# Kernel tuning notes

Hardware: AMD Instinct MI355X
Metric: run time of the kernel (lower is better)

Reference implementation:

```python
import jax, jax.numpy as jnp
import numpy as np

B, H, W, C = 8, 32, 32, 512
NUM_HEADS = 8
NUM_GROUPS = 32
EPS = 1e-5
SKIP_SCALE = 1.0
HEAD_DIM = C // NUM_HEADS


def setup_inputs() -> dict:
    key = jax.random.key(0)
    ks = jax.random.split(key, 7)
    fan_in, fan_out = C, 3 * C
    lim_qkv = np.sqrt(6.0 / (fan_in + fan_out))
    lim_out = 1e-5 * np.sqrt(6.0 / (C + C))
    return {
        "x": jax.random.normal(ks[0], (B, H, W, C), jnp.float32),
        "norm_scale": jnp.ones((C,), jnp.float32),
        "norm_bias": jnp.zeros((C,), jnp.float32),
        "qkv_kernel": jax.random.uniform(ks[1], (C, NUM_HEADS, 3 * HEAD_DIM), jnp.float32, -lim_qkv, lim_qkv),
        "qkv_bias": jnp.zeros((NUM_HEADS, 3 * HEAD_DIM), jnp.float32),
        "out_kernel": jax.random.uniform(ks[2], (NUM_HEADS, HEAD_DIM, C), jnp.float32, -lim_out, lim_out),
        "out_bias": jnp.zeros((C,), jnp.float32),
    }


def group_norm(x, scale, bias):
    # x: (B, S, C); normalize per-group over (S, C//G), flax GroupNorm semantics
    b, s, c = x.shape
    g = NUM_GROUPS
    xg = x.reshape(b, s, g, c // g)
    mean = jnp.mean(xg, axis=(1, 3), keepdims=True)
    var = jnp.var(xg, axis=(1, 3), keepdims=True)
    xg = (xg - mean) * jax.lax.rsqrt(var + EPS)
    return xg.reshape(b, s, c) * scale + bias


def reference(x, norm_scale, norm_bias, qkv_kernel, qkv_bias, out_kernel, out_bias):
    batch_dims = x.shape[:-3]
    h, w, c = x.shape[-3:]
    xi = x.reshape(-1, h * w, c)  # (B, S, C)
    out = group_norm(xi, norm_scale, norm_bias)
    # QKV projection: (B,S,C) x (C, NH, 3*HD) -> (B,S,NH,3*HD)
    qkv = jnp.einsum('bsc,chd->bshd', out, qkv_kernel) + qkv_bias
    q, k, v = jnp.split(qkv, 3, axis=-1)  # each (B,S,NH,HD)
    scale = 1.0 / jnp.sqrt(jnp.sqrt(jnp.asarray(HEAD_DIM, jnp.float32)))
    q = q * scale
    k = k * scale
    attn = jnp.einsum('bqhd,bkhd->bhqk', q, k)
    attn = jax.nn.softmax(attn, axis=-1)
    o = jnp.einsum('bhqk,bkhd->bqhd', attn, v)
    o = jnp.einsum('bqhd,hdc->bqc', o, out_kernel) + out_bias
    o = (o + xi) * SKIP_SCALE
    return o.reshape((*batch_dims, h, w, c))
```

## Files before the change

kernel.cpp:

```cpp
#include <hip/hip_runtime.h>
#include <stdint.h>

typedef __attribute__((ext_vector_type(8))) short short8;
typedef __attribute__((ext_vector_type(4))) float f32x4;
typedef __attribute__((ext_vector_type(16))) float f32x16;
typedef __attribute__((ext_vector_type(4))) unsigned int u32x4;
typedef unsigned short u16;
typedef unsigned int u32;

#define NBATCH 8
#define SLEN 1024
#define CDIM 512
#define NHEADS 8
#define HDIM 64
#define MROWS (NBATCH*SLEN)
#define NQKV (NHEADS*3*HDIM)
#define QK_SCALE 0.35355339059327373f
#define Q_SCALE_L2E 0.18033688011111793f
#define DEFER_THR 11.541560327111707f

__device__ inline u16 f2bf(float f){
  union{float f; uint32_t i;} v; v.f=f;
  uint32_t r = v.i + 0x7fffu + ((v.i>>16)&1u);
  return (u16)(r>>16);
}

__device__ inline u32 pk2(float a, float b){
  u32 r;
  asm("v_cvt_pk_bf16_f32 %0, %1, %2" : "=v"(r) : "v"(a), "v"(b));
  return r;
}

__device__ inline float exp2r(float x){
  float r;
  asm("v_exp_f32 %0, %1" : "=v"(r) : "v"(x));
  return r;
}

__device__ __forceinline__ void gld16(const u16* g, u16* l){
  __builtin_amdgcn_global_load_lds(
    (const __attribute__((address_space(1))) void*)g,
    (__attribute__((address_space(3))) void*)l, 16, 0, 0);
}

__device__ __forceinline__ void prep_body(const float* __restrict__ w, u16* __restrict__ wt,
                                          int N, int blk, int t){
  int tk = blk / (N/64), tn = blk % (N/64);
  int k0 = tk*64, n0 = tn*64;
  __shared__ u16 lt[64][72];
  int row = t >> 2, slot = t & 3;
  const float* src = w + (size_t)(k0+row)*N + n0 + slot*16;
  #pragma unroll
  for (int j=0;j<16;++j)
    lt[row][slot*16+j] = f2bf(src[j]);
  __syncthreads();
  u16 tmp[16];
  #pragma unroll
  for (int j=0;j<16;++j) tmp[j] = lt[slot*16+j][row];
  *(u32x4*)(wt + (size_t)(n0+row)*512 + k0 + slot*16)     = *(u32x4*)tmp;
  *(u32x4*)(wt + (size_t)(n0+row)*512 + k0 + slot*16 + 8) = *(u32x4*)(tmp+8);
}

__global__ __launch_bounds__(256) void prep_all(const float* __restrict__ wqkv, const float* __restrict__ wout,
                                                u16* __restrict__ wqkv_t, u16* __restrict__ wout_t){
  int blk = blockIdx.x, t = threadIdx.x;
  if (blk < 8*(NQKV/64)) prep_body(wqkv, wqkv_t, NQKV, blk, t);
  else                   prep_body(wout, wout_t, CDIM, blk - 8*(NQKV/64), t);
}

__global__ __launch_bounds__(512, 2) void gn_fused(const float* __restrict__ x,
                        const float* __restrict__ scale, const float* __restrict__ bias,
                        u16* __restrict__ xn){
  int bid = blockIdx.x;
  int b = bid >> 5, g = bid & 31;
  int t = threadIdx.x;
  const float* base = x + (size_t)b*SLEN*CDIM + g*16;
  u16* obase = xn + (size_t)b*SLEN*CDIM + g*16;
  float s1=0.f, s2=0.f;
  for (int s = t; s < SLEN; s += 512){
    const float4* p = (const float4*)(base + (size_t)s*CDIM);
    #pragma unroll
    for (int j=0;j<4;++j){
      float4 v = p[j];
      s1 += v.x+v.y+v.z+v.w;
      s2 += v.x*v.x + v.y*v.y + v.z*v.z + v.w*v.w;
    }
  }
  #pragma unroll
  for (int m=1;m<64;m<<=1){ s1 += __shfl_xor(s1,m); s2 += __shfl_xor(s2,m); }
  __shared__ float red[16];
  __shared__ float mv[2];
  int wid = t>>6;
  if ((t&63)==0){ red[wid*2]=s1; red[wid*2+1]=s2; }
  __syncthreads();
  if (t==0){
    float a=0,c=0;
    #pragma unroll
    for (int w2=0;w2<8;++w2){ a+=red[w2*2]; c+=red[w2*2+1]; }
    float mean = a*(1.f/16384.f);
    float var  = c*(1.f/16384.f) - mean*mean;
    mv[0] = mean; mv[1] = rsqrtf(var + 1e-5f);
  }
  __syncthreads();
  float mean = mv[0], rstd = mv[1];
  float sc[16], bi[16];
  #pragma unroll
  for (int j=0;j<16;++j){ sc[j] = scale[g*16+j]*rstd; bi[j] = bias[g*16+j] - mean*scale[g*16+j]*rstd; }
  for (int s = t; s < SLEN; s += 512){
    const float* xp = base + (size_t)s*CDIM;
    short8 o0, o1;
    #pragma unroll
    for (int j=0;j<16;++j){
      float v = xp[j]*sc[j] + bi[j];
      if (j<8) o0[j] = (short)f2bf(v); else o1[j-8] = (short)f2bf(v);
    }
    short8* dst = (short8*)(obase + (size_t)s*CDIM);
    dst[0]=o0; dst[1]=o1;
  }
}

#define BM 128
#define BN 128
#define BK 64

template<int EPI, int NT>
__global__ __launch_bounds__(256, 3) void gemm_bf16(
    const u16* __restrict__ A, const u16* __restrict__ Bt,
    const float* __restrict__ bias, const float* __restrict__ resid,
    float* __restrict__ outF,
    u16* __restrict__ qb, u16* __restrict__ kb, u16* __restrict__ vtb)
{
  const int K = CDIM;
  int t = threadIdx.x;
  int l = t & 63, wid = t >> 6;
  int g = l >> 4, c = l & 15;
  int wr = wid >> 1, wc = wid & 1;
  int nwg = gridDim.x;
  int cpx = nwg >> 3;
  int orig = blockIdx.x;
  int swz = (orig & 7)*cpx + (orig >> 3);
  int m0 = (swz / NT) * BM, n0 = (swz % NT) * BN;

  __shared__ __attribute__((aligned(16))) u16 ls[16384];
  char* lsAc = (char*)ls; char* lsBc = (char*)(ls + 8192);

  f32x4 acc[4][4];
  #pragma unroll
  for (int i=0;i<4;++i)
    #pragma unroll
    for(int j=0;j<4;++j) acc[i][j] = (f32x4)0.f;

  int lrow = l >> 3, slot = l & 7;
  int scol = ((slot ^ lrow) << 3);
  const int KT = K / BK;
  for (int kt=0; kt<KT; ++kt){
    __syncthreads();
    int kbo = kt*BK;
    #pragma unroll
    for (int q2=0; q2<4; ++q2){
      int row = wid*32 + q2*8 + lrow;
      gld16(A  + (size_t)(m0+row)*K + kbo + scol, ls        + (wid*4+q2)*512);
      gld16(Bt + (size_t)(n0+row)*K + kbo + scol, ls + 8192 + (wid*4+q2)*512);
    }
    asm volatile("s_waitcnt vmcnt(0)" ::: "memory");
    __syncthreads();
    #pragma unroll
    for (int kk=0; kk<2; ++kk){
      short8 af[4], bfr[4];
      #pragma unroll
      for (int i=0;i<4;++i){
        int rowA = wr*64 + i*16 + c;
        af[i]  = *(const short8*)(lsAc + rowA*128 + ((kk*4+g) ^ (rowA&7))*16);
        int rowB = wc*64 + i*16 + c;
        bfr[i] = *(const short8*)(lsBc + rowB*128 + ((kk*4+g) ^ (rowB&7))*16);
      }
      #pragma unroll
      for (int i=0;i<4;++i)
        #pragma unroll
        for (int j=0;j<4;++j)
          acc[i][j] = __builtin_amdgcn_mfma_f32_16x16x32_bf16(af[i], bfr[j], acc[i][j], 0,0,0);
    }
  }

  if (EPI == 0){
    int b = m0 >> 10, s0 = m0 & (SLEN-1);
    __syncthreads();
    u16* lsC = ls;
    #pragma unroll
    for (int i=0;i<4;++i){
      int rl0 = wr*64 + i*16 + g*4;
      #pragma unroll
      for (int j=0;j<4;++j){
        int cl = wc*64 + j*16 + c;
        int gcol = n0 + cl;
        int jj = gcol % 192;
        float sc_ = (jj < 64) ? Q_SCALE_L2E : 1.0f;
        float bv = bias[gcol];
        #pragma unroll
        for (int r=0;r<4;++r)
          lsC[(rl0+r)*128 + cl] = f2bf((acc[i][j][r] + bv)*sc_);
      }
    }
    __syncthreads();
    #pragma unroll
    for (int cc=0; cc<8; ++cc){
      int ch = cc*256 + t;
      int rl = ch >> 4, slot2 = ch & 15;
      int cl = slot2*8;
      int gcol = n0 + cl;
      int h = gcol / 192, jj = gcol % 192;
      int s = s0 + rl;
      u32x4 vv = *(const u32x4*)(lsC + rl*128 + cl);
      size_t rowb = ((size_t)(b*NHEADS+h))*SLEN + s;
      if (jj < 64)       __builtin_nontemporal_store(vv, (u32x4*)(qb + rowb*HDIM + jj));
      else if (jj < 128) __builtin_nontemporal_store(vv, (u32x4*)(kb + rowb*HDIM + (jj-64)));
    }
    int blk3 = (n0 >> 7) % 3;
    if (blk3 != 0){
      __syncthreads();
      u16* lsV = ls;
      #pragma unroll
      for (int i=0;i<4;++i){
        int rl0 = wr*64 + i*16 + g*4;
        #pragma unroll
        for (int j=0;j<4;++j){
          int cl = wc*64 + j*16 + c;
          int jj = (n0 + cl) % 192;
          if (jj >= 128){
            #pragma unroll
            for (int r=0;r<4;++r)
              lsV[(jj-128)*136 + rl0 + r] = f2bf(acc[i][j][r] + bias[n0+cl]);
          }
        }
      }
      __syncthreads();
      int hv = (n0 + ((blk3==1)?0:64)) / 192;
      size_t vbase = ((size_t)(b*NHEADS+hv))*HDIM*SLEN;
      #pragma unroll
      for (int cc=0; cc<4; ++cc){
        int chunk = cc*256 + t;
        int d = chunk >> 4, so = (chunk & 15)*8;
        u32x4 vv = *(const u32x4*)(lsV + d*136 + so);
        __builtin_nontemporal_store(vv, (u32x4*)(vtb + vbase + (size_t)d*SLEN + s0 + so));
      }
    }
  } else {
    #pragma unroll
    for (int i=0;i<4;++i){
      int grow = m0 + wr*64 + i*16 + g*4;
      #pragma unroll
      for (int j=0;j<4;++j){
        int gcol = n0 + wc*64 + j*16 + c;
        float bv = bias[gcol];
        #pragma unroll
        for (int r=0;r<4;++r){
          size_t off = (size_t)(grow+r)*CDIM + gcol;
          float rv = __builtin_nontemporal_load(&resid[off]);
          __builtin_nontemporal_store(acc[i][j][r] + bv + rv, &outF[off]);
        }
      }
    }
  }
}

#define PV_KS(PT, QOFF, V0, V1, KS, OA, OB) { \
    u32 A0 = pk2(PT[QOFF+0], PT[QOFF+1]); \
    u32 A1 = pk2(PT[QOFF+2], PT[QOFF+3]); \
    u32 B0 = pk2(PT[QOFF+4], PT[QOFF+5]); \
    u32 B1 = pk2(PT[QOFF+6], PT[QOFF+7]); \
    auto r0_ = __builtin_amdgcn_permlane32_swap((int)A0, (int)B0, false, false); \
    auto r1_ = __builtin_amdgcn_permlane32_swap((int)A1, (int)B1, false, false); \
    uint4 w; \
    w.x = (u32)r0_[0]; w.y = (u32)r1_[0]; w.z = (u32)r0_[1]; w.w = (u32)r1_[1]; \
    short8 fP; __builtin_memcpy(&fP, &w, 16); \
    OA = __builtin_amdgcn_mfma_f32_32x32x16_bf16(V0[KS], fP, OA, 0,0,0); \
    OB = __builtin_amdgcn_mfma_f32_32x32x16_bf16(V1[KS], fP, OB, 0,0,0); }

__global__ __launch_bounds__(256, 2) void attn_fused(const u16* __restrict__ qg,
  const u16* __restrict__ kg, const u16* __restrict__ vtg, u16* __restrict__ og)
{
  int bid = blockIdx.x;
  int nid = (bid & 7)*64 + (bid >> 3);
  int bh = nid >> 3, qi = nid & 7;
  int t = threadIdx.x, l = t & 63, wid = t >> 6;
  int q = l & 31, hi = l >> 5;
  int q0 = qi*128 + wid*32;

  __shared__ __attribute__((aligned(16))) u16 kl[4][4096];
  __shared__ __attribute__((aligned(16))) u16 vl[4][4096];

  const u16* qrow = qg + ((size_t)bh*SLEN + q0 + q)*HDIM + hi*8;
  short8 fQ[4];
  #pragma unroll
  for (int ds=0; ds<4; ++ds) fQ[ds] = *(const short8*)(qrow + ds*16);

  f32x16 o0a, o0b, o1a, o1b;
  #pragma unroll
  for (int r=0;r<16;++r){ o0a[r]=0.f; o0b[r]=0.f; o1a[r]=0.f; o1b[r]=0.f; }
  float mr = -1e30f, lsum = 0.f;

  const u16* kt_base = kg  + (size_t)bh*SLEN*HDIM;
  const u16* vt_base = vtg + (size_t)bh*HDIM*SLEN;
  int srow = l >> 3, sslot = l & 7;
  int scol8 = ((sslot ^ srow) << 3);

#define STAGE(BUF, KV) { \
    _Pragma("unroll") \
    for (int j=0;j<2;++j){ \
      int row = wid*16 + j*8 + srow; \
      int chunk = wid*2 + j; \
      gld16(kt_base + (size_t)((KV)*64 + row)*HDIM + scol8, &kl[BUF][chunk*512]); \
      gld16(vt_base + (size_t)row*SLEN + (KV)*64 + scol8,   &vl[BUF][chunk*512]); \
    } }

  STAGE(0, 0)
  STAGE(1, 1)
  STAGE(2, 2)
  STAGE(3, 3)

  int sl_q = q & 7;
  for (int p=0; p<8; ++p){
    if (p < 7) asm volatile("s_waitcnt vmcnt(8)" ::: "memory");
    else       asm volatile("s_waitcnt vmcnt(0)" ::: "memory");
    __syncthreads();
    int tA = 2*p, tB = 2*p+1;
    const u16* kA = &kl[tA&3][0]; const u16* kB = &kl[tB&3][0];
    const u16* vA = &vl[tA&3][0]; const u16* vB = &vl[tB&3][0];
    short8 fKA0[4], fKA1[4], fKB0[4], fKB1[4];
    #pragma unroll
    for (int ds=0; ds<4; ++ds){
      int sl = ((ds*2+hi) ^ sl_q) << 3;
      fKA0[ds] = *(const short8*)(kA + q*64 + sl);
      fKA1[ds] = *(const short8*)(kA + (q+32)*64 + sl);
      fKB0[ds] = *(const short8*)(kB + q*64 + sl);
      fKB1[ds] = *(const short8*)(kB + (q+32)*64 + sl);
    }
    f32x16 pA0, pA1, pB0, pB1;
    #pragma unroll
    for (int r=0;r<16;++r){ pA0[r]=0.f; pA1[r]=0.f; pB0[r]=0.f; pB1[r]=0.f; }
    __builtin_amdgcn_s_setprio(1);
    #pragma unroll
    for (int ds=0; ds<4; ++ds){
      pA0 = __builtin_amdgcn_mfma_f32_32x32x16_bf16(fKA0[ds], fQ[ds], pA0, 0,0,0);
      pB0 = __builtin_amdgcn_mfma_f32_32x32x16_bf16(fKB0[ds], fQ[ds], pB0, 0,0,0);
      pA1 = __builtin_amdgcn_mfma_f32_32x32x16_bf16(fKA1[ds], fQ[ds], pA1, 0,0,0);
      pB1 = __builtin_amdgcn_mfma_f32_32x32x16_bf16(fKB1[ds], fQ[ds], pB1, 0,0,0);
    }
    __builtin_amdgcn_s_setprio(0);
    short8 fVA0[4], fVA1[4], fVB0[4], fVB1[4];
    #pragma unroll
    for (int ks=0; ks<4; ++ks){
      int sl = ((ks*2+hi) ^ sl_q) << 3;
      fVA0[ks] = *(const short8*)(vA + q*64 + sl);
      fVA1[ks] = *(const short8*)(vA + (q+32)*64 + sl);
      fVB0[ks] = *(const short8*)(vB + q*64 + sl);
      fVB1[ks] = *(const short8*)(vB + (q+32)*64 + sl);
    }
    float a8[8];
    #pragma unroll
    for (int r=0;r<8;++r){
      float ma = fmaxf(fmaxf(pA0[r],pA0[r+8]), fmaxf(pA1[r],pA1[r+8]));
      float mb = fmaxf(fmaxf(pB0[r],pB0[r+8]), fmaxf(pB1[r],pB1[r+8]));
      a8[r] = fmaxf(ma, mb);
    }
    #pragma unroll
    for (int s=4;s>0;s>>=1)
      #pragma unroll
      for (int r=0;r<4;++r) if (r<s) a8[r] = fmaxf(a8[r], a8[r+s]);
    auto rm_ = __builtin_amdgcn_permlane32_swap(
        __builtin_bit_cast(int, a8[0]), __builtin_bit_cast(int, a8[0]), false, false);
    float tmax = fmaxf(a8[0], fmaxf(__builtin_bit_cast(float, rm_[0]),
                                    __builtin_bit_cast(float, rm_[1])));
    if (!__all(tmax <= mr + DEFER_THR)){
      float mn = fmaxf(mr, tmax);
      float alpha = exp2r(mr - mn);
      mr = mn;
      lsum *= alpha;
      #pragma unroll
      for (int r=0;r<16;++r){ o0a[r]*=alpha; o0b[r]*=alpha; o1a[r]*=alpha; o1b[r]*=alpha; }
    }
    #pragma unroll
    for (int r=0;r<16;++r){
      pA0[r] = exp2r(pA0[r]-mr); pA1[r] = exp2r(pA1[r]-mr);
      pB0[r] = exp2r(pB0[r]-mr); pB1[r] = exp2r(pB1[r]-mr);
    }
    float s8[8];
    #pragma unroll
    for (int r=0;r<8;++r)
      s8[r] = ((pA0[r]+pA0[r+8]) + (pA1[r]+pA1[r+8]))
            + ((pB0[r]+pB0[r+8]) + (pB1[r]+pB1[r+8]));
    #pragma unroll
    for (int s=4;s>0;s>>=1)
      #pragma unroll
      for (int r=0;r<4;++r) if (r<s) s8[r] += s8[r+s];
    auto rs_ = __builtin_amdgcn_permlane32_swap(
        __builtin_bit_cast(int, s8[0]), __builtin_bit_cast(int, s8[0]), false, false);
    lsum += __builtin_bit_cast(float, rs_[0]) + __builtin_bit_cast(float, rs_[1]);
    __builtin_amdgcn_s_setprio(1);
    PV_KS(pA0, 0, fVA0, fVA1, 0, o0a, o1a)
    PV_KS(pA0, 8, fVA0, fVA1, 1, o0a, o1a)
    PV_KS(pA1, 0, fVA0, fVA1, 2, o0b, o1b)
    PV_KS(pA1, 8, fVA0, fVA1, 3, o0b, o1b)
    PV_KS(pB0, 0, fVB0, fVB1, 0, o0a, o1a)
    PV_KS(pB0, 8, fVB0, fVB1, 1, o0a, o1a)
    PV_KS(pB1, 0, fVB0, fVB1, 2, o0b, o1b)
    PV_KS(pB1, 8, fVB0, fVB1, 3, o0b, o1b)
    __builtin_amdgcn_s_setprio(0);
    __syncthreads();
    if (p < 6){
      STAGE((2*p+4)&3, 2*p+4)
      STAGE((2*p+5)&3, 2*p+5)
    }
  }

  float inv = 1.f / lsum;
  int b = bh >> 3, h = bh & 7;
  u16* obase = og + ((size_t)b*SLEN + q0 + q)*CDIM + h*HDIM;
  #pragma unroll
  for (int pr=0; pr<8; ++pr){
    int d = ((2*pr)&3) + 8*(pr>>1) + 4*hi;
    *(u32*)(obase + d)      = pk2((o0a[2*pr]+o0b[2*pr])*inv, (o0a[2*pr+1]+o0b[2*pr+1])*inv);
    *(u32*)(obase + 32 + d) = pk2((o1a[2*pr]+o1b[2*pr])*inv, (o1a[2*pr+1]+o1b[2*pr+1])*inv);
  }
}

extern "C" void kernel_launch(void* const* d_in, const int* in_sizes, int n_in,
                              void* d_out, int out_size, void* d_ws, size_t ws_size,
                              hipStream_t stream){
  const float* x      = (const float*)d_in[0];
  const float* nscale = (const float*)d_in[1];
  const float* nbias  = (const float*)d_in[2];
  const float* wqkv   = (const float*)d_in[3];
  const float* bqkv   = (const float*)d_in[4];
  const float* wout   = (const float*)d_in[5];
  const float* bout   = (const float*)d_in[6];
  float* out = (float*)d_out;

  char* ws = (char*)d_ws;
  size_t off = 0;
  auto alloc = [&](size_t bytes){ void* p = ws + off; off += (bytes + 255) & ~255ull; return p; };
  u16* wqkv_t = (u16*)alloc((size_t)NQKV*CDIM*2);
  u16* wout_t = (u16*)alloc((size_t)CDIM*CDIM*2);
  u16* xn     = (u16*)alloc((size_t)MROWS*CDIM*2);
  u16* qb     = (u16*)alloc((size_t)MROWS*CDIM*2);
  u16* kb     = (u16*)alloc((size_t)MROWS*CDIM*2);
  u16* vtb    = (u16*)alloc((size_t)MROWS*CDIM*2);
  u16* ob     = (u16*)alloc((size_t)MROWS*CDIM*2);

  prep_all<<<dim3(8*(NQKV/64) + 8*(CDIM/64)), dim3(256), 0, stream>>>(wqkv, wout, wqkv_t, wout_t);
  gn_fused<<<dim3(256), dim3(512), 0, stream>>>(x, nscale, nbias, xn);
  gemm_bf16<0,12><<<dim3(768), dim3(256), 0, stream>>>(xn, wqkv_t, bqkv, nullptr, nullptr, qb, kb, vtb);
  attn_fused<<<dim3(512), dim3(256), 0, stream>>>(qb, kb, vtb, ob);
  gemm_bf16<1,4><<<dim3(256), dim3(256), 0, stream>>>(ob, wout_t, bout, x, out, nullptr, nullptr, nullptr);
}
```

Measured before the change: 91.94 us.

## Fuse weight prep with group norm; defer softmax row-sum reduction to epilogue

Merges the weight transpose/convert kernel and the group-norm kernel into one launch of 512-thread blocks, with the prep body reworked for 512 threads (8 elements per thread). In the attention kernel, the per-tile cross-lane softmax row-sum reduction is replaced by a per-lane 16-wide accumulator that is rescaled alongside the output and reduced only once after the loop. This removes one kernel launch and the per-iteration shuffle and permlane reduction work, at the cost of 16 extra VGPRs in the attention kernel, which may hurt occupancy.

```diff
diff --git a/kernel.cpp b/kernel.cpp
--- a/kernel.cpp
+++ b/kernel.cpp
@@ -15,9 +15,9 @@
 #define HDIM 64
 #define MROWS (NBATCH*SLEN)
 #define NQKV (NHEADS*3*HDIM)
-#define QK_SCALE 0.35355339059327373f
 #define Q_SCALE_L2E 0.18033688011111793f
 #define DEFER_THR 11.541560327111707f
+#define NPREP (8*(NQKV/64) + 8*(CDIM/64))
 
 __device__ inline u16 f2bf(float f){
   union{float f; uint32_t i;} v; v.f=f;
@@ -48,32 +48,31 @@
   int tk = blk / (N/64), tn = blk % (N/64);
   int k0 = tk*64, n0 = tn*64;
   __shared__ u16 lt[64][72];
-  int row = t >> 2, slot = t & 3;
-  const float* src = w + (size_t)(k0+row)*N + n0 + slot*16;
-  #pragma unroll
-  for (int j=0;j<16;++j)
-    lt[row][slot*16+j] = f2bf(src[j]);
+  int row = t >> 3, slot = t & 7;
+  const float* src = w + (size_t)(k0+row)*N + n0 + slot*8;
+  #pragma unroll
+  for (int j=0;j<8;++j)
+    lt[row][slot*8+j] = f2bf(src[j]);
   __syncthreads();
-  u16 tmp[16];
-  #pragma unroll
-  for (int j=0;j<16;++j) tmp[j] = lt[slot*16+j][row];
-  *(u32x4*)(wt + (size_t)(n0+row)*512 + k0 + slot*16)     = *(u32x4*)tmp;
-  *(u32x4*)(wt + (size_t)(n0+row)*512 + k0 + slot*16 + 8) = *(u32x4*)(tmp+8);
-}
-
-__global__ __launch_bounds__(256) void prep_all(const float* __restrict__ wqkv, const float* __restrict__ wout,
-                                                u16* __restrict__ wqkv_t, u16* __restrict__ wout_t){
+  u16 tmp[8];
+  #pragma unroll
+  for (int j=0;j<8;++j) tmp[j] = lt[slot*8+j][row];
+  *(u32x4*)(wt + (size_t)(n0+row)*512 + k0 + slot*8) = *(u32x4*)tmp;
+}
+
+__global__ __launch_bounds__(512) void pre_fused(
+    const float* __restrict__ wqkv, const float* __restrict__ wout,
+    u16* __restrict__ wqkv_t, u16* __restrict__ wout_t,
+    const float* __restrict__ x, const float* __restrict__ scale,
+    const float* __restrict__ bias, u16* __restrict__ xn){
   int blk = blockIdx.x, t = threadIdx.x;
-  if (blk < 8*(NQKV/64)) prep_body(wqkv, wqkv_t, NQKV, blk, t);
-  else                   prep_body(wout, wout_t, CDIM, blk - 8*(NQKV/64), t);
-}
-
-__global__ __launch_bounds__(512, 2) void gn_fused(const float* __restrict__ x,
-                        const float* __restrict__ scale, const float* __restrict__ bias,
-                        u16* __restrict__ xn){
-  int bid = blockIdx.x;
+  if (blk < NPREP){
+    if (blk < 8*(NQKV/64)) prep_body(wqkv, wqkv_t, NQKV, blk, t);
+    else                   prep_body(wout, wout_t, CDIM, blk - 8*(NQKV/64), t);
+    return;
+  }
+  int bid = blk - NPREP;
   int b = bid >> 5, g = bid & 31;
-  int t = threadIdx.x;
   const float* base = x + (size_t)b*SLEN*CDIM + g*16;
   u16* obase = xn + (size_t)b*SLEN*CDIM + g*16;
   float s1=0.f, s2=0.f;
@@ -294,10 +293,10 @@
   #pragma unroll
   for (int ds=0; ds<4; ++ds) fQ[ds] = *(const short8*)(qrow + ds*16);
 
-  f32x16 o0a, o0b, o1a, o1b;
-  #pragma unroll
-  for (int r=0;r<16;++r){ o0a[r]=0.f; o0b[r]=0.f; o1a[r]=0.f; o1b[r]=0.f; }
-  float mr = -1e30f, lsum = 0.f;
+  f32x16 o0a, o0b, o1a, o1b, ssum;
+  #pragma unroll
+  for (int r=0;r<16;++r){ o0a[r]=0.f; o0b[r]=0.f; o1a[r]=0.f; o1b[r]=0.f; ssum[r]=0.f; }
+  float mr = -1e30f;
 
   const u16* kt_base = kg  + (size_t)bh*SLEN*HDIM;
   const u16* vt_base = vtg + (size_t)bh*HDIM*SLEN;
@@ -375,27 +374,20 @@
       float mn = fmaxf(mr, tmax);
       float alpha = exp2r(mr - mn);
       mr = mn;
-      lsum *= alpha;
-      #pragma unroll
-      for (int r=0;r<16;++r){ o0a[r]*=alpha; o0b[r]*=alpha; o1a[r]*=alpha; o1b[r]*=alpha; }
+      #pragma unroll
+      for (int r=0;r<16;++r){
+        ssum[r]*=alpha;
+        o0a[r]*=alpha; o0b[r]*=alpha; o1a[r]*=alpha; o1b[r]*=alpha;
+      }
     }
     #pragma unroll
     for (int r=0;r<16;++r){
       pA0[r] = exp2r(pA0[r]-mr); pA1[r] = exp2r(pA1[r]-mr);
       pB0[r] = exp2r(pB0[r]-mr); pB1[r] = exp2r(pB1[r]-mr);
     }
-    float s8[8];
-    #pragma unroll
-    for (int r=0;r<8;++r)
-      s8[r] = ((pA0[r]+pA0[r+8]) + (pA1[r]+pA1[r+8]))
-            + ((pB0[r]+pB0[r+8]) + (pB1[r]+pB1[r+8]));
-    #pragma unroll
-    for (int s=4;s>0;s>>=1)
-      #pragma unroll
-      for (int r=0;r<4;++r) if (r<s) s8[r] += s8[r+s];
-    auto rs_ = __builtin_amdgcn_permlane32_swap(
-        __builtin_bit_cast(int, s8[0]), __builtin_bit_cast(int, s8[0]), false, false);
-    lsum += __builtin_bit_cast(float, rs_[0]) + __builtin_bit_cast(float, rs_[1]);
+    #pragma unroll
+    for (int r=0;r<16;++r)
+      ssum[r] += (pA0[r]+pA1[r]) + (pB0[r]+pB1[r]);
     __builtin_amdgcn_s_setprio(1);
     PV_KS(pA0, 0, fVA0, fVA1, 0, o0a, o1a)
     PV_KS(pA0, 8, fVA0, fVA1, 1, o0a, o1a)
@@ -413,6 +405,16 @@
     }
   }
 
+  float s8[8];
+  #pragma unroll
+  for (int r=0;r<8;++r) s8[r] = ssum[r] + ssum[r+8];
+  #pragma unroll
+  for (int s=4;s>0;s>>=1)
+    #pragma unroll
+    for (int r=0;r<4;++r) if (r<s) s8[r] += s8[r+s];
+  auto rs_ = __builtin_amdgcn_permlane32_swap(
+      __builtin_bit_cast(int, s8[0]), __builtin_bit_cast(int, s8[0]), false, false);
+  float lsum = __builtin_bit_cast(float, rs_[0]) + __builtin_bit_cast(float, rs_[1]);
   float inv = 1.f / lsum;
   int b = bh >> 3, h = bh & 7;
   u16* obase = og + ((size_t)b*SLEN + q0 + q)*CDIM + h*HDIM;
@@ -447,8 +449,8 @@
   u16* vtb    = (u16*)alloc((size_t)MROWS*CDIM*2);
   u16* ob     = (u16*)alloc((size_t)MROWS*CDIM*2);
 
-  prep_all<<<dim3(8*(NQKV/64) + 8*(CDIM/64)), dim3(256), 0, stream>>>(wqkv, wout, wqkv_t, wout_t);
-  gn_fused<<<dim3(256), dim3(512), 0, stream>>>(x, nscale, nbias, xn);
+  pre_fused<<<dim3(NPREP + 256), dim3(512), 0, stream>>>(wqkv, wout, wqkv_t, wout_t,
+                                                         x, nscale, nbias, xn);
   gemm_bf16<0,12><<<dim3(768), dim3(256), 0, stream>>>(xn, wqkv_t, bqkv, nullptr, nullptr, qb, kb, vtb);
   attn_fused<<<dim3(512), dim3(256), 0, stream>>>(qb, kb, vtb, ob);
   gemm_bf16<1,4><<<dim3(256), dim3(256), 0, stream>>>(ob, wout_t, bout, x, out, nullptr, nullptr, nullptr);
```

Result: slower. 94.65 us (+2.9%).
